# Kernel tuning notes

Hardware: AMD Instinct MI355X
Metric: run time of the kernel (lower is better)

Reference implementation:

```python
import jax, jax.numpy as jnp
import numpy as np

N_NODES = 50000
N_EDGES = 800000
D_NODE = 64
D_EDGE = 64


def setup_inputs() -> dict:
    key = jax.random.key(0)
    ks = jax.random.split(key, 6)
    node_scalars = jax.random.normal(ks[0], (N_NODES, D_NODE), dtype=jnp.float32)
    edge_feats = jax.random.normal(ks[1], (N_EDGES, D_EDGE), dtype=jnp.float32)
    src_idxs = jax.random.randint(ks[2], (N_EDGES,), 0, N_NODES, dtype=jnp.int32)
    dst_idxs = jax.random.randint(ks[3], (N_EDGES,), 0, N_NODES, dtype=jnp.int32)
    in_dim = 2 * D_NODE + D_EDGE  # 192
    # He-ish init for the MLP weights
    W1 = jax.random.normal(ks[4], (in_dim, D_EDGE), dtype=jnp.float32) / np.sqrt(in_dim)
    b1 = jnp.zeros((D_EDGE,), dtype=jnp.float32)
    W2 = jax.random.normal(ks[5], (D_EDGE, D_EDGE), dtype=jnp.float32) / np.sqrt(D_EDGE)
    b2 = jnp.zeros((D_EDGE,), dtype=jnp.float32)
    ln_gamma = jnp.ones((D_EDGE,), dtype=jnp.float32)
    ln_beta = jnp.zeros((D_EDGE,), dtype=jnp.float32)
    return {
        "node_scalars": node_scalars,
        "edge_feats": edge_feats,
        "src_idxs": src_idxs,
        "dst_idxs": dst_idxs,
        "W1": W1,
        "b1": b1,
        "W2": W2,
        "b2": b2,
        "ln_gamma": ln_gamma,
        "ln_beta": ln_beta,
    }


def _layer_norm(x, gamma, beta, eps=1e-5):
    mu = jnp.mean(x, axis=-1, keepdims=True)
    var = jnp.mean(jnp.square(x - mu), axis=-1, keepdims=True)
    return (x - mu) * jax.lax.rsqrt(var + eps) * gamma + beta


def reference(node_scalars, edge_feats, src_idxs, dst_idxs, W1, b1, W2, b2, ln_gamma, ln_beta):
    # gather endpoint node features per edge and concat with edge feats -> [E, 2*Dn + De]
    mlp_in = jnp.concatenate(
        [node_scalars[src_idxs], node_scalars[dst_idxs], edge_feats], axis=-1
    )
    h = jax.nn.silu(mlp_in @ W1 + b1)
    h = jax.nn.silu(h @ W2 + b2)
    return _layer_norm(edge_feats + h, ln_gamma, ln_beta)
```

## Files before the change

### kernel.cpp

```cpp
#include <hip/hip_runtime.h>

#define NE 800000
#define D  64
#define K1 192
#define AST 200

typedef __bf16 bf16x4v __attribute__((ext_vector_type(4)));
typedef __bf16 bf16x8  __attribute__((ext_vector_type(8)));
typedef float  f32x4   __attribute__((ext_vector_type(4)));

__global__ void prep_weights(const float* __restrict__ W1,
                             const float* __restrict__ W2,
                             __bf16* __restrict__ ws) {
  int i = blockIdx.x * 256 + threadIdx.x;
  if (i < K1 * D) {
    int k = i >> 6, n = i & 63;
    ws[n * K1 + k] = (__bf16)W1[i];
  } else {
    int j = i - K1 * D;
    int k = j >> 6, n = j & 63;
    ws[K1 * D + n * D + k] = (__bf16)W2[j];
  }
}

__device__ __forceinline__ void wave_lds_fence() {
  __asm__ volatile("s_waitcnt lgkmcnt(0)" ::: "memory");
}

__device__ __forceinline__ float silu(float x) {
  return x * __builtin_amdgcn_rcpf(1.f + __expf(-x));
}

template <bool USE_WS>
__global__ __launch_bounds__(256, 3)
void edge_kernel(const float* __restrict__ nodes, const float* __restrict__ ef,
                 const int* __restrict__ srci, const int* __restrict__ dsti,
                 const float* __restrict__ W1, const float* __restrict__ b1,
                 const float* __restrict__ W2, const float* __restrict__ b2,
                 const float* __restrict__ gmm, const float* __restrict__ bta,
                 const __bf16* __restrict__ wsw, float* __restrict__ out) {
  __shared__ __align__(16) __bf16 w1t[64 * AST];
  __shared__ __align__(16) __bf16 atile_all[4][16 * AST];
  __shared__ float sb1[64], sb2[64], sg[64], sbt[64];

  const int tid = threadIdx.x;
  const int wave = tid >> 6, lane = tid & 63;
  const int quad = lane >> 4, m16 = lane & 15;

  if (USE_WS) {
    const uint2* s1 = (const uint2*)wsw;
    for (int c = tid; c < 3072; c += 256) {
      int n = c / 48, kc = c - n * 48;
      *(uint2*)&w1t[n * AST + kc * 4] = s1[c];
    }
  } else {
    for (int i = tid; i < K1 * D; i += 256) {
      int k = i >> 6, n = i & 63;
      w1t[n * AST + k] = (__bf16)W1[i];
    }
  }
  if (tid < 64)       sb1[tid]       = b1[tid];
  else if (tid < 128) sb2[tid - 64]  = b2[tid - 64];
  else if (tid < 192) sg[tid - 128]  = gmm[tid - 128];
  else                sbt[tid - 192] = bta[tid - 192];

  bf16x8 w2f[2][4];
  if (USE_WS) {
    const __bf16* w2t = wsw + K1 * D;
    #pragma unroll
    for (int ki = 0; ki < 2; ++ki)
      #pragma unroll
      for (int nt = 0; nt < 4; ++nt)
        w2f[ki][nt] = *(const bf16x8*)&w2t[(nt * 16 + m16) * 64 + ki * 32 + quad * 8];
  } else {
    #pragma unroll
    for (int ki = 0; ki < 2; ++ki)
      #pragma unroll
      for (int nt = 0; nt < 4; ++nt) {
        const int n = nt * 16 + m16;
        #pragma unroll
        for (int j = 0; j < 8; ++j)
          w2f[ki][nt][j] = (__bf16)W2[(ki * 32 + quad * 8 + j) * 64 + n];
      }
  }
  __syncthreads();

  __bf16* At = atile_all[wave];
  float*  Af = (float*)At;

  #pragma unroll 1
  for (int t = 0; t < 4; ++t) {
    const int base = blockIdx.x * 256 + wave * 64 + t * 16;

    int si[4], di[4];
    #pragma unroll
    for (int i = 0; i < 4; ++i) {
      si[i] = srci[base + i * 4 + quad];
      di[i] = dsti[base + i * 4 + quad];
    }
    #pragma unroll
    for (int i = 0; i < 4; ++i) {
      const int row = i * 4 + quad;
      f32x4 sv = *(const f32x4*)(nodes + (size_t)si[i] * D + m16 * 4);
      f32x4 dv = *(const f32x4*)(nodes + (size_t)di[i] * D + m16 * 4);
      f32x4 ev = *(const f32x4*)(ef + (size_t)(base + row) * D + m16 * 4);
      bf16x4v sb, db, eb;
      #pragma unroll
      for (int j = 0; j < 4; ++j) {
        sb[j] = (__bf16)sv[j]; db[j] = (__bf16)dv[j]; eb[j] = (__bf16)ev[j];
      }
      *(bf16x4v*)&At[row * AST +       m16 * 4] = sb;
      *(bf16x4v*)&At[row * AST +  64 + m16 * 4] = db;
      *(bf16x4v*)&At[row * AST + 128 + m16 * 4] = eb;
    }
    wave_lds_fence();

    f32x4 acc[4] = {};
    #pragma unroll
    for (int ki = 0; ki < 6; ++ki) {
      bf16x8 a = *(const bf16x8*)&At[m16 * AST + ki * 32 + quad * 8];
      #pragma unroll
      for (int nt = 0; nt < 4; ++nt) {
        bf16x8 bfv = *(const bf16x8*)&w1t[(nt * 16 + m16) * AST + ki * 32 + quad * 8];
        acc[nt] = __builtin_amdgcn_mfma_f32_16x16x32_bf16(a, bfv, acc[nt], 0, 0, 0);
      }
    }

    #pragma unroll
    for (int nt = 0; nt < 4; ++nt) {
      const int c = nt * 16 + m16;
      const float bb = sb1[c];
      #pragma unroll
      for (int r = 0; r < 4; ++r)
        At[(quad * 4 + r) * AST + c] = (__bf16)silu(acc[nt][r] + bb);
    }
    wave_lds_fence();

    f32x4 acc2[4] = {};
    #pragma unroll
    for (int ki = 0; ki < 2; ++ki) {
      bf16x8 a = *(const bf16x8*)&At[m16 * AST + ki * 32 + quad * 8];
      #pragma unroll
      for (int nt = 0; nt < 4; ++nt)
        acc2[nt] = __builtin_amdgcn_mfma_f32_16x16x32_bf16(a, w2f[ki][nt], acc2[nt], 0, 0, 0);
    }

    #pragma unroll
    for (int r = 0; r < 4; ++r) {
      const int row = quad * 4 + r;
      float x[4];
      float sum = 0.f;
      #pragma unroll
      for (int nt = 0; nt < 4; ++nt) {
        const int c = nt * 16 + m16;
        float h = silu(acc2[nt][r] + sb2[c]);
        float efv = (float)At[row * AST + 128 + c];
        x[nt] = efv + h;
        sum += x[nt];
      }
      float sq = x[0] * x[0] + x[1] * x[1] + x[2] * x[2] + x[3] * x[3];
      #pragma unroll
      for (int off = 1; off < 16; off <<= 1) {
        sum += __shfl_xor(sum, off);
        sq  += __shfl_xor(sq, off);
      }
      const float mean = sum * (1.f / 64.f);
      const float var  = sq * (1.f / 64.f) - mean * mean;
      const float rstd = rsqrtf(var + 1e-5f);
      #pragma unroll
      for (int nt = 0; nt < 4; ++nt) {
        const int c = nt * 16 + m16;
        Af[row * (AST / 2) + c] = (x[nt] - mean) * rstd * sg[c] + sbt[c];
      }
    }
    wave_lds_fence();

    #pragma unroll
    for (int i = 0; i < 4; ++i) {
      const int row = i * 4 + quad;
      f32x4 ov = *(const f32x4*)&Af[row * (AST / 2) + m16 * 4];
      *(f32x4*)(out + (size_t)(base + row) * D + m16 * 4) = ov;
    }
    wave_lds_fence();
  }
}

extern "C" void kernel_launch(void* const* d_in, const int* in_sizes, int n_in,
                              void* d_out, int out_size, void* d_ws, size_t ws_size,
                              hipStream_t stream) {
  const float* nodes = (const float*)d_in[0];
  const float* ef    = (const float*)d_in[1];
  const int*   srci  = (const int*)d_in[2];
  const int*   dsti  = (const int*)d_in[3];
  const float* W1    = (const float*)d_in[4];
  const float* b1    = (const float*)d_in[5];
  const float* W2    = (const float*)d_in[6];
  const float* b2    = (const float*)d_in[7];
  const float* gmm   = (const float*)d_in[8];
  const float* bta   = (const float*)d_in[9];
  float* out = (float*)d_out;

  const int blocks = NE / 256;
  if (ws_size >= (size_t)(K1 * D + D * D) * 2) {
    prep_weights<<<64, 256, 0, stream>>>(W1, W2, (__bf16*)d_ws);
    edge_kernel<true><<<blocks, 256, 0, stream>>>(
        nodes, ef, srci, dsti, W1, b1, W2, b2, gmm, bta,
        (const __bf16*)d_ws, out);
  } else {
    edge_kernel<false><<<blocks, 256, 0, stream>>>(
        nodes, ef, srci, dsti, W1, b1, W2, b2, gmm, bta, nullptr, out);
  }
}
```

Before: 402.0 us.

## Prefetch next tile's gathered node and edge features during compute

Loads all 16 src/dst indices per lane up front, then software-pipelines the per-tile gathers so the next tile's node and edge feature loads are issued before the current tile's MFMA and epilogue work. The loop is fully unrolled. The goal is to hide global gather latency behind compute in this memory-bound kernel. The cost is higher register pressure: 32 index registers plus 48 floats of prefetch buffers, under launch bounds of 3 blocks per CU. That could force spills or lower occupancy.

```diff
diff --git a/kernel.cpp b/kernel.cpp
--- a/kernel.cpp
+++ b/kernel.cpp
@@ -88,30 +88,51 @@
   __bf16* At = atile_all[wave];
   float*  Af = (float*)At;
 
-  #pragma unroll 1
+  const int wbase = blockIdx.x * 256 + wave * 64;
+
+  int si[4][4], di[4][4];
+  #pragma unroll
+  for (int t = 0; t < 4; ++t)
+    #pragma unroll
+    for (int i = 0; i < 4; ++i) {
+      si[t][i] = srci[wbase + t * 16 + i * 4 + quad];
+      di[t][i] = dsti[wbase + t * 16 + i * 4 + quad];
+    }
+
+  f32x4 sv[4], dv[4], ev[4];
+  #pragma unroll
+  for (int i = 0; i < 4; ++i) {
+    const int row = i * 4 + quad;
+    sv[i] = *(const f32x4*)(nodes + (size_t)si[0][i] * D + m16 * 4);
+    dv[i] = *(const f32x4*)(nodes + (size_t)di[0][i] * D + m16 * 4);
+    ev[i] = *(const f32x4*)(ef + (size_t)(wbase + row) * D + m16 * 4);
+  }
+
+  #pragma unroll
   for (int t = 0; t < 4; ++t) {
-    const int base = blockIdx.x * 256 + wave * 64 + t * 16;
-
-    int si[4], di[4];
-    #pragma unroll
-    for (int i = 0; i < 4; ++i) {
-      si[i] = srci[base + i * 4 + quad];
-      di[i] = dsti[base + i * 4 + quad];
-    }
+    const int base = wbase + t * 16;
+
     #pragma unroll
     for (int i = 0; i < 4; ++i) {
       const int row = i * 4 + quad;
-      f32x4 sv = *(const f32x4*)(nodes + (size_t)si[i] * D + m16 * 4);
-      f32x4 dv = *(const f32x4*)(nodes + (size_t)di[i] * D + m16 * 4);
-      f32x4 ev = *(const f32x4*)(ef + (size_t)(base + row) * D + m16 * 4);
       bf16x4v sb, db, eb;
       #pragma unroll
       for (int j = 0; j < 4; ++j) {
-        sb[j] = (__bf16)sv[j]; db[j] = (__bf16)dv[j]; eb[j] = (__bf16)ev[j];
+        sb[j] = (__bf16)sv[i][j]; db[j] = (__bf16)dv[i][j]; eb[j] = (__bf16)ev[i][j];
       }
       *(bf16x4v*)&At[row * AST +       m16 * 4] = sb;
       *(bf16x4v*)&At[row * AST +  64 + m16 * 4] = db;
       *(bf16x4v*)&At[row * AST + 128 + m16 * 4] = eb;
+    }
+
+    if (t < 3) {
+      #pragma unroll
+      for (int i = 0; i < 4; ++i) {
+        const int row = i * 4 + quad;
+        sv[i] = *(const f32x4*)(nodes + (size_t)si[t + 1][i] * D + m16 * 4);
+        dv[i] = *(const f32x4*)(nodes + (size_t)di[t + 1][i] * D + m16 * 4);
+        ev[i] = *(const f32x4*)(ef + (size_t)(base + 16 + row) * D + m16 * 4);
+      }
     }
     wave_lds_fence();
 
```

Result: slower. 420.9 us (+4.7%).
